# Kernel tuning notes

Hardware: AMD Instinct MI355X
Metric: run time of the kernel (lower is better)

The kernel has to match this reference:

```python
import jax, jax.numpy as jnp
import numpy as np

B, P = 4, 2048
NUM_MODS, D_TIME = 22, 8
DIM_S = NUM_MODS + D_TIME + 1          # 31
PHI_W, PSI_W, PSI_LAT = 32, 32, 32
DOT, HEADS, RHO_W = 16, 4, 64


def _xavier(key, shape):
    fan_in, fan_out = shape[0], shape[1]
    std = (2.0 / (fan_in + fan_out)) ** 0.5
    return jax.random.normal(key, shape, jnp.float32) * std


def setup_inputs() -> dict:
    key = jax.random.key(0)
    ks = jax.random.split(key, 20)
    inp = {
        "times": jnp.sort(jax.random.uniform(ks[0], (B, P), jnp.float32) * 100.0, axis=1),
        "values": jax.random.normal(ks[1], (B, P), jnp.float32),
        "measurements": jax.random.randint(ks[2], (B, P), 0, NUM_MODS + 1, jnp.int64 if jax.config.jax_enable_x64 else jnp.int32),
        "non_pad_mask": jnp.ones((B, P, 1), jnp.float32),
        # attention.psi MLP_state(dim_s -> psi_width)
        "psi_w1": _xavier(ks[3], (DIM_S, PSI_W)), "psi_b1": jnp.zeros((PSI_W,), jnp.float32),
        "psi_w2": _xavier(ks[4], (PSI_W, PSI_W)), "psi_b2": jnp.zeros((PSI_W,), jnp.float32),
        # attention.rho Linear(psi_width -> psi_latent_width)
        "arho_w": _xavier(ks[5], (PSI_W, PSI_LAT)), "arho_b": jnp.zeros((PSI_LAT,), jnp.float32),
        # attention key/query projections
        "W_k": _xavier(ks[6], (PSI_LAT + DIM_S, DOT * HEADS)),
        "W_q": _xavier(ks[7], (HEADS, DOT)),
        # phi MLP_state(dim_s -> phi_width)
        "phi_w1": _xavier(ks[8], (DIM_S, PHI_W)), "phi_b1": jnp.zeros((PHI_W,), jnp.float32),
        "phi_w2": _xavier(ks[9], (PHI_W, PHI_W)), "phi_b2": jnp.zeros((PHI_W,), jnp.float32),
        # rho MLP_state(n_heads*phi_width -> rho_width)
        "rho_w1": _xavier(ks[10], (HEADS * PHI_W, RHO_W)), "rho_b1": jnp.zeros((RHO_W,), jnp.float32),
        "rho_w2": _xavier(ks[11], (RHO_W, RHO_W)), "rho_b2": jnp.zeros((RHO_W,), jnp.float32),
    }
    return inp


def _mlp_state(x, mask, w1, b1, w2, b2):
    # MLP_state: relu(fc1(x*mask)); relu(fc2(h*mask)); h*mask  (dropout p=0)
    h = jax.nn.relu((x * mask) @ w1 + b1)
    h = jax.nn.relu((h * mask) @ w2 + b2)
    return h * mask


def _forward(times, values, measurements, non_pad_mask,
             psi_w1, psi_b1, psi_w2, psi_b2, arho_w, arho_b, W_k, W_q,
             phi_w1, phi_b1, phi_w2, phi_b2, rho_w1, rho_b1, rho_w2, rho_b2):
    mask = non_pad_mask  # [B,P,1]
    # temporal encoding: time / 10000^(2*(i//2)/d_time), sin on even, cos on odd
    idx = jnp.arange(D_TIME)
    pos_vec = jnp.power(10000.0, 2.0 * (idx // 2).astype(jnp.float32) / D_TIME)
    r = times[:, :, None] / pos_vec[None, None, :]          # [B,P,d_time]
    tenc = jnp.where(idx % 2 == 0, jnp.sin(r), jnp.cos(r))
    # one-hot measurements, drop padding channel 0
    meas = jax.nn.one_hot(measurements, NUM_MODS + 1, dtype=jnp.float32)[:, :, 1:]
    combined = jnp.concatenate([tenc, values[:, :, None], meas], axis=-1)  # [B,P,dim_s]

    # --- CumulativeSetAttentionLayer ---
    enc_psi = _mlp_state(combined, mask, psi_w1, psi_b1, psi_w2, psi_b2)   # [B,P,psi_w]
    counts = jnp.arange(1, P + 1, dtype=jnp.float32)[None, :, None]
    agg = jnp.cumsum(enc_psi, axis=1) / counts * mask                      # cumulative mean
    agg = (agg @ arho_w + arho_b) * mask                                   # [B,P,psi_lat]
    comb2 = jnp.concatenate([combined, agg], axis=-1)                      # [B,P,dim_s+psi_lat]
    keys = (comb2 @ W_k) * mask                                            # [B,P,DOT*HEADS]
    # torch.split(keys, n_heads, -1) + stack(-1): chunk i has size HEADS -> [B,P,HEADS,DOT]
    keys = keys.reshape(B, P, DOT, HEADS).transpose(0, 1, 3, 2)            # [B,P,h,d]
    preattn = jnp.einsum('bphd,hd->bph', keys, W_q) / jnp.sqrt(jnp.float32(DOT))
    preattn = preattn * mask                                               # [B,P,m]

    # --- phi encoding ---
    enc = _mlp_state(combined, mask, phi_w1, phi_b1, phi_w2, phi_b2)       # [B,P,d_phi]

    # --- cumulative causal softmax weighting ---
    A = preattn[:, None, :, :]                                             # [B,1,Q,m]
    Bc = jax.lax.cummax(preattn, axis=1)[:, :, None, :]                    # [B,P,1,m]
    triu = jnp.triu(jnp.ones((P, P), bool), 1)[None, :, :, None]           # mask Q > P
    D = jnp.exp(jnp.where(triu, -jnp.inf, A - Bc))                          # [B,P,Q,m]
    E = jnp.sum(D, axis=2)                                                 # [B,P,m]
    out5 = jnp.einsum('bpqm,bqd->bpmd', D, enc) / E[:, :, :, None]
    out5 = out5 * mask[:, :, :, None]                                      # [B,P,m,d_phi]

    agg2 = out5.reshape(B, P, HEADS * PHI_W)
    output = _mlp_state(agg2, mask, rho_w1, rho_b1, rho_w2, rho_b2)        # [B,P,rho_w]
    return output


def reference(times, values, measurements, non_pad_mask,
              psi_w1, psi_b1, psi_w2, psi_b2, arho_w, arho_b, W_k, W_q,
              phi_w1, phi_b1, phi_w2, phi_b2, rho_w1, rho_b1, rho_w2, rho_b2):
    return _forward(times, values, measurements, non_pad_mask,
                    psi_w1, psi_b1, psi_w2, psi_b2, arho_w, arho_b, W_k, W_q,
                    phi_w1, phi_b1, phi_w2, phi_b2, rho_w1, rho_b1, rho_w2, rho_b2)
```

## Files before the change

### kernel.cpp

```cpp
#include <hip/hip_runtime.h>
#include <math.h>

#define PB 2048
#define OFF_ENC 0
#define OFF_Q   262144
#define OFF_R   294912
#define OFF_MSK 327680
#define OFF_WV  335872

__global__ __launch_bounds__(64) void k_encode(
    const float* __restrict__ times, const float* __restrict__ vals,
    const int* __restrict__ meas, const float* __restrict__ mask,
    const float* __restrict__ psi_w1, const float* __restrict__ psi_b1,
    const float* __restrict__ psi_w2, const float* __restrict__ psi_b2,
    const float* __restrict__ phi_w1, const float* __restrict__ phi_b1,
    const float* __restrict__ phi_w2, const float* __restrict__ phi_b2,
    const float* __restrict__ arho_w, const float* __restrict__ arho_b,
    const float* __restrict__ W_k, const float* __restrict__ W_q,
    float* __restrict__ ws)
{
    __shared__ float sW[4222];
    __shared__ float sU[31*4];
    __shared__ float sU2[32*4];
    __shared__ float sV[32*4];
    __shared__ float sCc[4];
    for (int i = threadIdx.x; i < 1023; i += 64) {
        int r = i / 33, cc = i - r * 33;
        sW[i]        = (cc < 32) ? psi_w1[r*32 + cc] : 0.0f;
        sW[2111 + i] = (cc < 32) ? phi_w1[r*32 + cc] : 0.0f;
    }
    for (int i = threadIdx.x; i < 1024; i += 64) {
        sW[1055 + i] = psi_w2[i];
        sW[3166 + i] = phi_w2[i];
    }
    if (threadIdx.x < 32) {
        int i = threadIdx.x;
        sW[1023 + i] = psi_b1[i];
        sW[2079 + i] = psi_b2[i];
        sW[3134 + i] = phi_b1[i];
        sW[4190 + i] = phi_b2[i];
    }
    for (int t = threadIdx.x; t < 252; t += 64) {
        int i = t >> 2, h = t & 3;
        float s = 0.0f;
        #pragma unroll
        for (int d = 0; d < 16; d++)
            s = fmaf(W_k[i*64 + d*4 + h], W_q[h*16 + d], s);
        s *= 0.25f;
        if (i < 31) sU[i*4 + h] = s; else sU2[(i-31)*4 + h] = s;
    }
    __syncthreads();
    for (int t = threadIdx.x; t < 128; t += 64) {
        int ch = t >> 2, h = t & 3;
        float s = 0.0f;
        #pragma unroll
        for (int j = 0; j < 32; j++)
            s = fmaf(arho_w[ch*32 + j], sU2[j*4 + h], s);
        sV[t] = s;
    }
    if (threadIdx.x < 4) {
        float s = 0.0f;
        #pragma unroll
        for (int j = 0; j < 32; j++)
            s = fmaf(arho_b[j], sU2[j*4 + threadIdx.x], s);
        sCc[threadIdx.x] = s;
    }
    __syncthreads();

    const int pp = blockIdx.x * 64 + threadIdx.x;
    const int b = pp >> 11, p = pp & 2047;
    const float t = times[pp];
    const float v = vals[pp];
    const float msk = mask[pp];
    const int m = meas[pp];

    float c[9];
    c[0] = sinf(t);           c[1] = cosf(t);
    c[2] = sinf(t * 0.1f);    c[3] = cosf(t * 0.1f);
    c[4] = sinf(t * 0.01f);   c[5] = cosf(t * 0.01f);
    c[6] = sinf(t * 0.001f);  c[7] = cosf(t * 0.001f);
    c[8] = v;

    float* enc_t = ws + OFF_ENC;
    const int cb = b * 32;

    float x[9];
    #pragma unroll
    for (int i = 0; i < 9; i++) x[i] = c[i] * msk;
    const float ohs = (m > 0) ? msk : 0.0f;
    const int   ohr = (m > 0) ? (8 + m) * 33 : 0;

    float r[4] = {sCc[0], sCc[1], sCc[2], sCc[3]};
    #pragma unroll
    for (int i = 0; i < 9; i++) {
        #pragma unroll
        for (int h = 0; h < 4; h++) r[h] = fmaf(c[i], sU[i*4 + h], r[h]);
    }
    if (m > 0) {
        #pragma unroll
        for (int h = 0; h < 4; h++) r[h] += sU[(8 + m)*4 + h];
    }
    #pragma unroll
    for (int h = 0; h < 4; h++)
        ws[OFF_R + (size_t)(b*4 + h) * PB + p] = r[h];
    ws[OFF_MSK + (size_t)b * PB + p] = msk;

    {
        float h1[32];
        #pragma unroll
        for (int j = 0; j < 32; j++) {
            float acc = sW[1023 + j];
            #pragma unroll
            for (int i = 0; i < 9; i++) acc = fmaf(x[i], sW[i*33 + j], acc);
            acc = fmaf(ohs, sW[ohr + j], acc);
            h1[j] = fmaxf(acc, 0.0f) * msk;
        }
        float q[4] = {0.f, 0.f, 0.f, 0.f};
        #pragma unroll
        for (int j = 0; j < 32; j++) {
            float acc = sW[2079 + j];
            #pragma unroll
            for (int i = 0; i < 32; i++) acc = fmaf(h1[i], sW[1055 + i*32 + j], acc);
            const float p2 = fmaxf(acc, 0.0f) * msk;
            #pragma unroll
            for (int h = 0; h < 4; h++) q[h] = fmaf(p2, sV[j*4 + h], q[h]);
        }
        #pragma unroll
        for (int h = 0; h < 4; h++)
            ws[OFF_Q + (size_t)(b*4 + h) * PB + p] = q[h];
    }
    {
        float h1[32];
        #pragma unroll
        for (int j = 0; j < 32; j++) {
            float acc = sW[3134 + j];
            #pragma unroll
            for (int i = 0; i < 9; i++) acc = fmaf(x[i], sW[2111 + i*33 + j], acc);
            acc = fmaf(ohs, sW[2111 + ohr + j], acc);
            h1[j] = fmaxf(acc, 0.0f) * msk;
        }
        #pragma unroll
        for (int j = 0; j < 32; j++) {
            float acc = sW[4190 + j];
            #pragma unroll
            for (int i = 0; i < 32; i++) acc = fmaf(h1[i], sW[3166 + i*32 + j], acc);
            enc_t[(size_t)(cb + j) * PB + p] = fmaxf(acc, 0.0f) * msk;
        }
    }
}

__global__ __launch_bounds__(64) void k_mid(float* __restrict__ ws)
{
    const int blk = blockIdx.x;
    const int bh = blk / 33;
    const int c  = blk - bh * 33;
    const int b  = bh >> 2;
    const int lane = threadIdx.x;

    const float4* q4 = (const float4*)(ws + OFF_Q   + (size_t)bh * PB + lane * 32);
    const float4* r4 = (const float4*)(ws + OFF_R   + (size_t)bh * PB + lane * 32);
    const float4* m4 = (const float4*)(ws + OFF_MSK + (size_t)b  * PB + lane * 32);
    const float4* e4 = (const float4*)(ws + OFF_ENC + ((size_t)(b*32 + (c-1))) * PB + lane * 32);
    float4* o4 = (float4*)(ws + OFF_WV + ((size_t)(bh*33 + c)) * PB + lane * 32);

    float vq[32];
    #pragma unroll
    for (int k = 0; k < 8; k++) {
        float4 f = q4[k];
        vq[4*k] = f.x; vq[4*k+1] = f.y; vq[4*k+2] = f.z; vq[4*k+3] = f.w;
    }
    #pragma unroll
    for (int j = 1; j < 32; j++) vq[j] += vq[j-1];
    {
        const float tot = vq[31];
        float x = tot;
        #pragma unroll
        for (int off = 1; off < 64; off <<= 1) {
            float y = __shfl_up(x, off);
            if (lane >= off) x += y;
        }
        const float excl = x - tot;
        #pragma unroll
        for (int j = 0; j < 32; j++) vq[j] += excl;
    }
    float v[32];
    #pragma unroll
    for (int k = 0; k < 8; k++) {
        const float4 fr = r4[k];
        const float4 fm = m4[k];
        const int p0 = lane * 32 + 4*k;
        v[4*k+0] = expf(fm.x * (fr.x + vq[4*k+0] / (float)(p0 + 1)));
        v[4*k+1] = expf(fm.y * (fr.y + vq[4*k+1] / (float)(p0 + 2)));
        v[4*k+2] = expf(fm.z * (fr.z + vq[4*k+2] / (float)(p0 + 3)));
        v[4*k+3] = expf(fm.w * (fr.w + vq[4*k+3] / (float)(p0 + 4)));
    }
    if (c > 0) {
        #pragma unroll
        for (int k = 0; k < 8; k++) {
            float4 f = e4[k];
            v[4*k] *= f.x; v[4*k+1] *= f.y; v[4*k+2] *= f.z; v[4*k+3] *= f.w;
        }
    }
    #pragma unroll
    for (int j = 1; j < 32; j++) v[j] += v[j-1];
    const float tot = v[31];
    float x = tot;
    #pragma unroll
    for (int off = 1; off < 64; off <<= 1) {
        float y = __shfl_up(x, off);
        if (lane >= off) x += y;
    }
    const float excl = x - tot;
    #pragma unroll
    for (int j = 0; j < 32; j++) v[j] += excl;
    #pragma unroll
    for (int k = 0; k < 8; k++)
        o4[k] = make_float4(v[4*k], v[4*k+1], v[4*k+2], v[4*k+3]);
}

__global__ __launch_bounds__(256) void k_rho(
    const float* __restrict__ rho_w1, const float* __restrict__ rho_b1,
    const float* __restrict__ rho_w2, const float* __restrict__ rho_b2,
    const float* __restrict__ ws, float* __restrict__ out)
{
    __shared__ float h1s[16][65];
    __shared__ float scl[16][4];
    __shared__ float mskS[16];
    const int tid = threadIdx.x;
    const int pos = tid >> 4;
    const int g   = tid & 15;
    const int pbase = blockIdx.x * 16;
    const int b  = pbase >> 11;
    const int p0 = pbase & 2047;
    const float* wv = ws + OFF_WV + (size_t)b * 132 * PB;

    if (tid < 64) {
        const int pp = tid >> 2, h = tid & 3;
        const float msk = ws[OFF_MSK + (size_t)b * PB + p0 + pp];
        const float L = wv[(size_t)(h*33) * PB + p0 + pp];
        scl[pp][h] = msk / L;
        if (h == 0) mskS[pp] = msk;
    }
    __syncthreads();

    const int pg = p0 + pos;
    float4 acc = ((const float4*)rho_b1)[g];
    const float4* w14 = (const float4*)rho_w1;
    const float sc0 = scl[pos][0], sc1 = scl[pos][1];
    const float sc2 = scl[pos][2], sc3 = scl[pos][3];
    #pragma unroll
    for (int h = 0; h < 4; h++) {
        const float sc = (h == 0) ? sc0 : (h == 1) ? sc1 : (h == 2) ? sc2 : sc3;
        const float* wvh = wv + (size_t)(h*33 + 1) * PB + pg;
        #pragma unroll 8
        for (int d = 0; d < 32; d++) {
            const float ai = wvh[(size_t)d * PB] * sc;
            const float4 w = w14[(h*32 + d)*16 + g];
            acc.x = fmaf(ai, w.x, acc.x);
            acc.y = fmaf(ai, w.y, acc.y);
            acc.z = fmaf(ai, w.z, acc.z);
            acc.w = fmaf(ai, w.w, acc.w);
        }
    }
    const float msk = mskS[pos];
    h1s[pos][g*4+0] = fmaxf(acc.x, 0.f) * msk;
    h1s[pos][g*4+1] = fmaxf(acc.y, 0.f) * msk;
    h1s[pos][g*4+2] = fmaxf(acc.z, 0.f) * msk;
    h1s[pos][g*4+3] = fmaxf(acc.w, 0.f) * msk;
    __syncthreads();

    float4 acc2 = ((const float4*)rho_b2)[g];
    const float4* w24 = (const float4*)rho_w2;
    #pragma unroll 16
    for (int i = 0; i < 64; i++) {
        const float hv = h1s[pos][i];
        const float4 w = w24[i*16 + g];
        acc2.x = fmaf(hv, w.x, acc2.x);
        acc2.y = fmaf(hv, w.y, acc2.y);
        acc2.z = fmaf(hv, w.z, acc2.z);
        acc2.w = fmaf(hv, w.w, acc2.w);
    }
    float4 o;
    o.x = fmaxf(acc2.x, 0.f) * msk;
    o.y = fmaxf(acc2.y, 0.f) * msk;
    o.z = fmaxf(acc2.z, 0.f) * msk;
    o.w = fmaxf(acc2.w, 0.f) * msk;
    ((float4*)out)[(size_t)(pbase + pos) * 16 + g] = o;
}

extern "C" void kernel_launch(void* const* d_in, const int* in_sizes, int n_in,
                              void* d_out, int out_size, void* d_ws, size_t ws_size,
                              hipStream_t stream)
{
    const float* times  = (const float*)d_in[0];
    const float* vals   = (const float*)d_in[1];
    const int*   meas   = (const int*)d_in[2];
    const float* mask   = (const float*)d_in[3];
    const float* psi_w1 = (const float*)d_in[4];
    const float* psi_b1 = (const float*)d_in[5];
    const float* psi_w2 = (const float*)d_in[6];
    const float* psi_b2 = (const float*)d_in[7];
    const float* arho_w = (const float*)d_in[8];
    const float* arho_b = (const float*)d_in[9];
    const float* W_k    = (const float*)d_in[10];
    const float* W_q    = (const float*)d_in[11];
    const float* phi_w1 = (const float*)d_in[12];
    const float* phi_b1 = (const float*)d_in[13];
    const float* phi_w2 = (const float*)d_in[14];
    const float* phi_b2 = (const float*)d_in[15];
    const float* rho_w1 = (const float*)d_in[16];
    const float* rho_b1 = (const float*)d_in[17];
    const float* rho_w2 = (const float*)d_in[18];
    const float* rho_b2 = (const float*)d_in[19];
    float* ws  = (float*)d_ws;
    float* out = (float*)d_out;

    k_encode<<<dim3(128), dim3(64), 0, stream>>>(times, vals, meas, mask,
        psi_w1, psi_b1, psi_w2, psi_b2, phi_w1, phi_b1, phi_w2, phi_b2,
        arho_w, arho_b, W_k, W_q, ws);
    k_mid<<<dim3(528), dim3(64), 0, stream>>>(ws);
    k_rho<<<dim3(512), dim3(256), 0, stream>>>(rho_w1, rho_b1, rho_w2, rho_b2, ws, out);
}
```

Baseline: 139.9 us.

## Split encode MLP output channels across two half-waves with lane shuffles

The encode kernel now gives each point to two 32-lane halves of a wave, and each half computes 16 of the 32 hidden and output channels. The halves swap first-layer activations with cross-half shuffles and sum the partial attention-query results, and the grid doubles to 256 blocks. The goal is more parallelism and less serial work per thread in a kernel that only had 128 single-wave blocks. In exchange, the scalar time features and the weight staging into shared memory are repeated in twice as many blocks, and shuffle overhead is added.

```diff
diff --git a/kernel.cpp b/kernel.cpp
--- a/kernel.cpp
+++ b/kernel.cpp
@@ -67,7 +67,10 @@
     }
     __syncthreads();
 
-    const int pp = blockIdx.x * 64 + threadIdx.x;
+    const int tid  = threadIdx.x;
+    const int half = tid >> 5;
+    const int jb   = half << 4;
+    const int pp = blockIdx.x * 32 + (tid & 31);
     const int b = pp >> 11, p = pp & 2047;
     const float t = times[pp];
     const float v = vals[pp];
@@ -90,60 +93,84 @@
     const float ohs = (m > 0) ? msk : 0.0f;
     const int   ohr = (m > 0) ? (8 + m) * 33 : 0;
 
-    float r[4] = {sCc[0], sCc[1], sCc[2], sCc[3]};
-    #pragma unroll
-    for (int i = 0; i < 9; i++) {
-        #pragma unroll
-        for (int h = 0; h < 4; h++) r[h] = fmaf(c[i], sU[i*4 + h], r[h]);
-    }
-    if (m > 0) {
-        #pragma unroll
-        for (int h = 0; h < 4; h++) r[h] += sU[(8 + m)*4 + h];
-    }
-    #pragma unroll
-    for (int h = 0; h < 4; h++)
-        ws[OFF_R + (size_t)(b*4 + h) * PB + p] = r[h];
-    ws[OFF_MSK + (size_t)b * PB + p] = msk;
+    if (half == 0) {
+        float r[4] = {sCc[0], sCc[1], sCc[2], sCc[3]};
+        #pragma unroll
+        for (int i = 0; i < 9; i++) {
+            #pragma unroll
+            for (int h = 0; h < 4; h++) r[h] = fmaf(c[i], sU[i*4 + h], r[h]);
+        }
+        if (m > 0) {
+            #pragma unroll
+            for (int h = 0; h < 4; h++) r[h] += sU[(8 + m)*4 + h];
+        }
+        #pragma unroll
+        for (int h = 0; h < 4; h++)
+            ws[OFF_R + (size_t)(b*4 + h) * PB + p] = r[h];
+        ws[OFF_MSK + (size_t)b * PB + p] = msk;
+    }
 
     {
-        float h1[32];
-        #pragma unroll
-        for (int j = 0; j < 32; j++) {
+        float h1o[16];
+        #pragma unroll
+        for (int jj = 0; jj < 16; jj++) {
+            const int j = jb + jj;
             float acc = sW[1023 + j];
             #pragma unroll
             for (int i = 0; i < 9; i++) acc = fmaf(x[i], sW[i*33 + j], acc);
             acc = fmaf(ohs, sW[ohr + j], acc);
-            h1[j] = fmaxf(acc, 0.0f) * msk;
+            h1o[jj] = fmaxf(acc, 0.0f) * msk;
+        }
+        float h1f[32];
+        #pragma unroll
+        for (int jj = 0; jj < 16; jj++) {
+            const float other = __shfl_xor(h1o[jj], 32);
+            h1f[jj]      = half ? other   : h1o[jj];
+            h1f[16 + jj] = half ? h1o[jj] : other;
         }
         float q[4] = {0.f, 0.f, 0.f, 0.f};
         #pragma unroll
-        for (int j = 0; j < 32; j++) {
+        for (int jj = 0; jj < 16; jj++) {
+            const int j = jb + jj;
             float acc = sW[2079 + j];
             #pragma unroll
-            for (int i = 0; i < 32; i++) acc = fmaf(h1[i], sW[1055 + i*32 + j], acc);
+            for (int i = 0; i < 32; i++) acc = fmaf(h1f[i], sW[1055 + i*32 + j], acc);
             const float p2 = fmaxf(acc, 0.0f) * msk;
             #pragma unroll
             for (int h = 0; h < 4; h++) q[h] = fmaf(p2, sV[j*4 + h], q[h]);
         }
         #pragma unroll
-        for (int h = 0; h < 4; h++)
-            ws[OFF_Q + (size_t)(b*4 + h) * PB + p] = q[h];
+        for (int h = 0; h < 4; h++) q[h] += __shfl_xor(q[h], 32);
+        if (half == 0) {
+            #pragma unroll
+            for (int h = 0; h < 4; h++)
+                ws[OFF_Q + (size_t)(b*4 + h) * PB + p] = q[h];
+        }
     }
     {
-        float h1[32];
-        #pragma unroll
-        for (int j = 0; j < 32; j++) {
+        float h1o[16];
+        #pragma unroll
+        for (int jj = 0; jj < 16; jj++) {
+            const int j = jb + jj;
             float acc = sW[3134 + j];
             #pragma unroll
             for (int i = 0; i < 9; i++) acc = fmaf(x[i], sW[2111 + i*33 + j], acc);
             acc = fmaf(ohs, sW[2111 + ohr + j], acc);
-            h1[j] = fmaxf(acc, 0.0f) * msk;
-        }
-        #pragma unroll
-        for (int j = 0; j < 32; j++) {
+            h1o[jj] = fmaxf(acc, 0.0f) * msk;
+        }
+        float h1f[32];
+        #pragma unroll
+        for (int jj = 0; jj < 16; jj++) {
+            const float other = __shfl_xor(h1o[jj], 32);
+            h1f[jj]      = half ? other   : h1o[jj];
+            h1f[16 + jj] = half ? h1o[jj] : other;
+        }
+        #pragma unroll
+        for (int jj = 0; jj < 16; jj++) {
+            const int j = jb + jj;
             float acc = sW[4190 + j];
             #pragma unroll
-            for (int i = 0; i < 32; i++) acc = fmaf(h1[i], sW[3166 + i*32 + j], acc);
+            for (int i = 0; i < 32; i++) acc = fmaf(h1f[i], sW[3166 + i*32 + j], acc);
             enc_t[(size_t)(cb + j) * PB + p] = fmaxf(acc, 0.0f) * msk;
         }
     }
@@ -315,7 +342,7 @@
     float* ws  = (float*)d_ws;
     float* out = (float*)d_out;
 
-    k_encode<<<dim3(128), dim3(64), 0, stream>>>(times, vals, meas, mask,
+    k_encode<<<dim3(256), dim3(64), 0, stream>>>(times, vals, meas, mask,
         psi_w1, psi_b1, psi_w2, psi_b2, phi_w1, phi_b1, phi_w2, phi_b2,
         arho_w, arho_b, W_k, W_q, ws);
     k_mid<<<dim3(528), dim3(64), 0, stream>>>(ws);
```

New measurement: 135.5 us. 1.03x faster.
